# Kernel optimization log

Hardware: AMD Instinct MI355X
Metric: run time of the kernel (lower is better)

Reference implementation:

```python
import jax, jax.numpy as jnp
import numpy as np

# dims: batch, sentences, p/q/a token lens, choices, hidden, selected sentences
B, N, P, Q, A, M, L, K = 32, 32, 64, 32, 24, 4, 768, 2
EPS = 1e-8


def _normalize(x):
    n = jnp.linalg.norm(x, axis=-1, keepdims=True)
    return x / jnp.maximum(n, EPS)


def setup_inputs() -> dict:
    key = jax.random.key(0)
    ks = jax.random.split(key, 16)
    w = lambda k, shape: jax.random.normal(k, shape, jnp.float32) * 0.02
    return {
        "H_p": jax.random.normal(ks[0], (B, N * P, L), jnp.float32),
        "H_q": jax.random.normal(ks[1], (B, Q, L), jnp.float32),
        "H_a": jax.random.normal(ks[2], (B, M * A, L), jnp.float32),
        "W5": w(ks[3], (L, L)),
        "W6": w(ks[4], ((M - 1) * L, L)),
        "W7": w(ks[5], (L, L)),
        "W8": w(ks[6], (L, L)),
        "b8": jnp.zeros((L,), jnp.float32),
        "W9": w(ks[7], (L, L)),
        "W10": w(ks[8], (L, L)),
        "W11": w(ks[9], (L, L)),
        "W12": w(ks[10], (L, L)),
        "W13": w(ks[11], (L, L)),
        "W14": w(ks[12], (L, L)),
        "b14": jnp.zeros((L,), jnp.float32),
        "V": w(ks[13], (3 * L, 1)),
    }


def reference(H_p, H_q, H_a, W5, W6, W7, W8, b8, W9, W10, W11, W12, W13, W14, b14, V):
    Bq = H_q.shape[0]
    Hp = H_p.reshape(Bq, N, P, L)   # (B, N, p, l)
    Ha = H_a.reshape(Bq, M, A, L)   # (B, m, a, l)

    # --- passage sentence selection (cosine scoring) ---
    # The torch code materializes O(B*m*N*a*p*l) repeated tensors; the math is just
    # pairwise cosine similarity -> max over passage tokens -> mean over a/q tokens.
    Pn, An, Qn = _normalize(Hp), _normalize(Ha), _normalize(H_q)
    sim_pa = jnp.einsum('bnpl,bmal->bmnap', Pn, An)  # (B, m, N, a, p)
    score_a = sim_pa.max(-1).mean(-1).sum(1)          # max over p, mean over a, sum over m -> (B, N)
    sim_pq = jnp.einsum('bnpl,bql->bnqp', Pn, Qn)     # (B, N, q, p)
    score_q = sim_pq.max(-1).mean(-1)                 # (B, N)
    score = score_a + score_q
    top_idx = jnp.argsort(-score, axis=-1)[:, :K]     # descending, top-K sentences
    H_p_s = jnp.take_along_axis(Hp, top_idx[:, :, None, None], axis=1).reshape(Bq, K * P, L)

    # --- answer option interaction ---
    H_o = []
    for i in range(M):
        Hi = Ha[:, i]                                  # (B, a, l)
        cache1 = Hi @ W5
        hats = []
        for j in range(M):
            if j != i:
                Hj = Ha[:, j]
                G = jax.nn.softmax(jnp.einsum('bal,bkl->bak', cache1, Hj), axis=-1)
                hats.append(jax.nn.relu(jnp.einsum('bak,bkl->bal', G, Hj)))
        bar = jnp.concatenate(hats, axis=-1) @ W6      # (B, a, l)
        g = jax.nn.sigmoid(bar @ W7 + bar @ W8 + b8)
        H_o.append(g * Hi + (1.0 - g) * bar)
    H_o = jnp.stack(H_o, axis=1)                       # (B, m, a, l)

    # --- bidirectional matching ---
    def match(Hx, Hy, Gxy_left, Gyx_left):
        Gxy = jax.nn.softmax(jnp.einsum('bxl,byl->bxy', Gxy_left, Hy), axis=-1)
        Gyx = jax.nn.softmax(jnp.einsum('byl,bxl->byx', Gyx_left, Hx), axis=-1)
        Ex = jnp.einsum('bxy,byl->bxl', Gxy, Hy)
        Ey = jnp.einsum('byx,bxl->byl', Gyx, Hx)
        Sxy = jax.nn.relu(Ex @ W11).max(1)             # (B, l)
        Syx = jax.nn.relu(Ey @ W12).max(1)             # (B, l)
        g = jax.nn.sigmoid(Sxy @ W13 + Syx @ W14 + b14)
        return g * Sxy + (1.0 - g) * Syx

    cache1 = H_p_s @ W9
    cache2 = H_q @ W9
    cache3 = H_q @ W10
    M_pq = match(H_p_s, H_q, cache1, cache3)
    C = []
    for i in range(M):
        Hoi = H_o[:, i]
        cache4 = Hoi @ W10
        M_po = match(H_p_s, Hoi, cache1, cache4)
        M_qo = match(H_q, Hoi, cache2, cache4)
        C.append(jnp.concatenate([M_pq, M_po, M_qo], axis=-1))
    C = jnp.stack(C, axis=1)                           # (B, m, 3l)
    logits = (C @ V).squeeze(-1)                       # (B, m)
    return jax.nn.log_softmax(logits, axis=-1)
```

## Files before the change

kernel.cpp:

```cpp
#include <hip/hip_runtime.h>
#include <math.h>


typedef __bf16 bf16x8 __attribute__((ext_vector_type(8)));
typedef float f32x4 __attribute__((ext_vector_type(4)));

__global__ void prep_kernel(const float* __restrict__ W5, const float* __restrict__ W6,
                            const float* __restrict__ W7, const float* __restrict__ W8,
                            const float* __restrict__ W9, const float* __restrict__ W10,
                            const float* __restrict__ W11, const float* __restrict__ W12,
                            const float* __restrict__ W13, const float* __restrict__ W14,
                            __bf16* __restrict__ W5t_h, __bf16* __restrict__ W5t_l,
                            __bf16* __restrict__ WsQT_h, __bf16* __restrict__ WsQT_l,
                            __bf16* __restrict__ W6t_h, __bf16* __restrict__ W6t_l,
                            __bf16* __restrict__ W1112T, __bf16* __restrict__ W78t,
                            __bf16* __restrict__ W1314t) {
    long i = (long)blockIdx.x * 256 + threadIdx.x;
    if (i < 589824) {
        int c = (int)(i / 768), r = (int)(i % 768);
        float v = W5[r * 768 + c];
        __bf16 h = (__bf16)v; W5t_h[i] = h; W5t_l[i] = (__bf16)(v - (float)h);
        return;
    } i -= 589824;
    if (i < 1179648) {
        int c = (int)(i / 768), r = (int)(i % 768);
        float v = (c < 768) ? W9[r * 768 + c] : W10[r * 768 + c - 768];
        __bf16 h = (__bf16)v; WsQT_h[i] = h; WsQT_l[i] = (__bf16)(v - (float)h);
        return;
    } i -= 1179648;
    if (i < 1769472) {
        int c = (int)(i / 2304), r = (int)(i % 2304);
        float v = W6[r * 768 + c];
        __bf16 h = (__bf16)v; W6t_h[i] = h; W6t_l[i] = (__bf16)(v - (float)h);
        return;
    } i -= 1769472;
    if (i < 1179648) {
        int c = (int)(i / 768), r = (int)(i % 768);
        W1112T[i] = (__bf16)((c < 768) ? W11[r * 768 + c] : W12[r * 768 + c - 768]);
        return;
    } i -= 1179648;
    if (i < 589824) {
        int c = (int)(i / 768), r = (int)(i % 768);
        W78t[i] = (__bf16)(W7[r * 768 + c] + W8[r * 768 + c]);
        return;
    } i -= 589824;
    if (i < 1179648) {
        int c = (int)(i / 1536), r = (int)(i % 1536);
        W1314t[i] = (__bf16)((r < 768) ? W13[r * 768 + c] : W14[(r - 768) * 768 + c]);
    }
}

__global__ void cvt2_kernel(const float* __restrict__ src, __bf16* __restrict__ h,
                            __bf16* __restrict__ l, long n) {
    long i = (long)blockIdx.x * 256 + threadIdx.x;
    if (i < n) {
        float v = src[i];
        __bf16 hv = (__bf16)v; h[i] = hv; l[i] = (__bf16)(v - (float)hv);
    }
}

__global__ void rnorm_kernel(const float* __restrict__ X, float* __restrict__ out) {
    long row = blockIdx.x;
    const float* xr = X + row * 768;
    int t = threadIdx.x;
    float ss = 0.f;
    for (int l = t; l < 768; l += 256) { float v = xr[l]; ss += v * v; }
    for (int o = 32; o; o >>= 1) ss += __shfl_xor(ss, o);
    __shared__ float red[4];
    if ((t & 63) == 0) red[t >> 6] = ss;
    __syncthreads();
    if (t == 0) {
        float tot = red[0] + red[1] + red[2] + red[3];
        out[row] = 1.f / fmaxf(sqrtf(tot), 1e-8f);
    }
}

__global__ __launch_bounds__(256) void simmax_kernel(
    const float* __restrict__ Hp,
    const __bf16* __restrict__ Ha_h, const __bf16* __restrict__ Ha_l,
    const __bf16* __restrict__ Hq_h, const __bf16* __restrict__ Hq_l,
    const float* __restrict__ ra, const float* __restrict__ rq,
    float* __restrict__ amax) {
    constexpr int LDT = 72;
    __shared__ alignas(16) __bf16 Ah[64 * LDT];
    __shared__ alignas(16) __bf16 Al[64 * LDT];
    __shared__ alignas(16) __bf16 Bh[128 * LDT];
    __shared__ alignas(16) __bf16 Bl[128 * LDT];
    __shared__ float rp_lds[64];
    __shared__ float wred[4][128];
    int b = blockIdx.x >> 5, n = blockIdx.x & 31;
    int t = threadIdx.x;
    const float* Ap = Hp + ((long)b * 2048 + n * 64) * 768;
    int srow = t >> 2, kq = (t & 3) << 4;
    int brow = t >> 1, kh = (t & 1) << 5;
    const __bf16 *Bsh, *Bsl;
    if (brow < 96) {
        Bsh = Ha_h + (long)b * 73728 + (long)brow * 768;
        Bsl = Ha_l + (long)b * 73728 + (long)brow * 768;
    } else {
        Bsh = Hq_h + (long)b * 24576 + (long)(brow - 96) * 768;
        Bsl = Hq_l + (long)b * 24576 + (long)(brow - 96) * 768;
    }
    int w = t >> 6, l = t & 63;
    int fr = l & 15, g = l >> 4;
    int wr = w << 4;
    f32x4 acc[8] = {};
    float ss = 0.f;
    const float* Arow = Ap + (long)srow * 768 + kq;
    for (int k0 = 0; k0 < 768; k0 += 64) {
        float4 av0 = *(const float4*)(Arow + k0 + 0);
        float4 av1 = *(const float4*)(Arow + k0 + 4);
        float4 av2 = *(const float4*)(Arow + k0 + 8);
        float4 av3 = *(const float4*)(Arow + k0 + 12);
        bf16x8 vbh0 = *(const bf16x8*)(Bsh + k0 + kh);
        bf16x8 vbh1 = *(const bf16x8*)(Bsh + k0 + kh + 8);
        bf16x8 vbh2 = *(const bf16x8*)(Bsh + k0 + kh + 16);
        bf16x8 vbh3 = *(const bf16x8*)(Bsh + k0 + kh + 24);
        bf16x8 vbl0 = *(const bf16x8*)(Bsl + k0 + kh);
        bf16x8 vbl1 = *(const bf16x8*)(Bsl + k0 + kh + 8);
        bf16x8 vbl2 = *(const bf16x8*)(Bsl + k0 + kh + 16);
        bf16x8 vbl3 = *(const bf16x8*)(Bsl + k0 + kh + 24);
        float va[16];
        *(float4*)(va + 0) = av0; *(float4*)(va + 4) = av1;
        *(float4*)(va + 8) = av2; *(float4*)(va + 12) = av3;
        bf16x8 h0, h1, l0, l1;
#pragma unroll
        for (int i = 0; i < 8; i++) {
            float v = va[i]; __bf16 hv = (__bf16)v;
            h0[i] = hv; l0[i] = (__bf16)(v - (float)hv); ss += v * v;
            v = va[8 + i]; hv = (__bf16)v;
            h1[i] = hv; l1[i] = (__bf16)(v - (float)hv); ss += v * v;
        }
        __syncthreads();
        *(bf16x8*)(&Ah[srow * LDT + kq]) = h0;
        *(bf16x8*)(&Ah[srow * LDT + kq + 8]) = h1;
        *(bf16x8*)(&Al[srow * LDT + kq]) = l0;
        *(bf16x8*)(&Al[srow * LDT + kq + 8]) = l1;
        *(bf16x8*)(&Bh[brow * LDT + kh]) = vbh0;
        *(bf16x8*)(&Bh[brow * LDT + kh + 8]) = vbh1;
        *(bf16x8*)(&Bh[brow * LDT + kh + 16]) = vbh2;
        *(bf16x8*)(&Bh[brow * LDT + kh + 24]) = vbh3;
        *(bf16x8*)(&Bl[brow * LDT + kh]) = vbl0;
        *(bf16x8*)(&Bl[brow * LDT + kh + 8]) = vbl1;
        *(bf16x8*)(&Bl[brow * LDT + kh + 16]) = vbl2;
        *(bf16x8*)(&Bl[brow * LDT + kh + 24]) = vbl3;
        __syncthreads();
#pragma unroll
        for (int sub = 0; sub < 2; sub++) {
            int kb = sub * 32 + g * 8;
            bf16x8 fah = *(const bf16x8*)(&Ah[(wr + fr) * LDT + kb]);
            bf16x8 fal = *(const bf16x8*)(&Al[(wr + fr) * LDT + kb]);
#pragma unroll
            for (int c = 0; c < 8; c++) {
                bf16x8 fbh = *(const bf16x8*)(&Bh[(c * 16 + fr) * LDT + kb]);
                bf16x8 fbl = *(const bf16x8*)(&Bl[(c * 16 + fr) * LDT + kb]);
                acc[c] = __builtin_amdgcn_mfma_f32_16x16x32_bf16(fah, fbh, acc[c], 0, 0, 0);
                acc[c] = __builtin_amdgcn_mfma_f32_16x16x32_bf16(fah, fbl, acc[c], 0, 0, 0);
                acc[c] = __builtin_amdgcn_mfma_f32_16x16x32_bf16(fal, fbh, acc[c], 0, 0, 0);
            }
        }
    }
    ss += __shfl_xor(ss, 1);
    ss += __shfl_xor(ss, 2);
    if ((t & 3) == 0) rp_lds[srow] = 1.f / fmaxf(sqrtf(ss), 1e-8f);
    __syncthreads();
    float rpv[4];
#pragma unroll
    for (int r = 0; r < 4; r++) rpv[r] = rp_lds[wr + g * 4 + r];
// ... 48 lines not shown
    __bf16 h = (__bf16)v; Hps_h[i] = h; Hps_l[i] = (__bf16)(v - (float)h);
}

template <int BIASF, int BOUT>
__global__ __launch_bounds__(256) void mgemm_kernel(
    const __bf16* __restrict__ A, int Kdim, int Mtot,
    const __bf16* __restrict__ Wt, const float* __restrict__ bias,
    float* __restrict__ C, int ldc, __bf16* __restrict__ Cb) {
    constexpr int LDT = 80;
    __shared__ alignas(16) __bf16 As[64 * LDT];
    __shared__ alignas(16) __bf16 Bs[64 * LDT];
    int t = threadIdx.x;
    int rowBase = blockIdx.x << 6, colBase = blockIdx.y << 6;
    int srow = t >> 2, skof = (t & 3) << 3;
    int arow = rowBase + srow;
    bool aok = arow < Mtot;
    const __bf16* Ap = A + (long)(aok ? arow : rowBase) * Kdim + skof;
    const __bf16* Wp = Wt + (long)(colBase + srow) * Kdim + skof;
    int w = t >> 6, l = t & 63;
    int wr = (w >> 1) << 5, wc = (w & 1) << 5;
    int fr = l & 15, g = l >> 4;
    f32x4 acc[2][2] = {};
    int nk = Kdim >> 6;
    for (int ks = 0; ks < nk; ks++) {
        bf16x8 a0 = *(const bf16x8*)(Ap);
        bf16x8 a1 = *(const bf16x8*)(Ap + 32);
        bf16x8 w0 = *(const bf16x8*)(Wp);
        bf16x8 w1 = *(const bf16x8*)(Wp + 32);
        Ap += 64; Wp += 64;
        __syncthreads();
        *(bf16x8*)(&As[srow * LDT + skof]) = a0;
        *(bf16x8*)(&As[srow * LDT + 32 + skof]) = a1;
        *(bf16x8*)(&Bs[srow * LDT + skof]) = w0;
        *(bf16x8*)(&Bs[srow * LDT + 32 + skof]) = w1;
        __syncthreads();
#pragma unroll
        for (int sub = 0; sub < 2; sub++) {
            int ko = sub * 32 + g * 8;
            bf16x8 fa0 = *(const bf16x8*)(&As[(wr + fr) * LDT + ko]);
            bf16x8 fa1 = *(const bf16x8*)(&As[(wr + 16 + fr) * LDT + ko]);
            bf16x8 fb0 = *(const bf16x8*)(&Bs[(wc + fr) * LDT + ko]);
            bf16x8 fb1 = *(const bf16x8*)(&Bs[(wc + 16 + fr) * LDT + ko]);
            acc[0][0] = __builtin_amdgcn_mfma_f32_16x16x32_bf16(fa0, fb0, acc[0][0], 0, 0, 0);
            acc[0][1] = __builtin_amdgcn_mfma_f32_16x16x32_bf16(fa0, fb1, acc[0][1], 0, 0, 0);
            acc[1][0] = __builtin_amdgcn_mfma_f32_16x16x32_bf16(fa1, fb0, acc[1][0], 0, 0, 0);
            acc[1][1] = __builtin_amdgcn_mfma_f32_16x16x32_bf16(fa1, fb1, acc[1][1], 0, 0, 0);
        }
    }
#pragma unroll
    for (int fi = 0; fi < 2; fi++)
#pragma unroll
    for (int fj = 0; fj < 2; fj++)
#pragma unroll
    for (int r = 0; r < 4; r++) {
        int row = rowBase + wr + fi * 16 + g * 4 + r;
        int col = colBase + wc + fj * 16 + (l & 15);
        if (row < Mtot) {
            float v = acc[fi][fj][r];
            if (BIASF) v += bias[col];
            if (BOUT == 0) C[(long)row * ldc + col] = v;
            else Cb[(long)row * ldc + col] = (__bf16)v;
        }
    }
}

template <int OUT>
__global__ __launch_bounds__(256) void mgemm3_kernel(
    const __bf16* __restrict__ Ah, const __bf16* __restrict__ Al, int Kdim, int Mtot,
    const __bf16* __restrict__ Wh, const __bf16* __restrict__ Wl,
    float* __restrict__ C, int ldc, __bf16* __restrict__ Ch, __bf16* __restrict__ Cl) {
    constexpr int LDT = 80;
    __shared__ alignas(16) __bf16 Ahs[64 * LDT];
    __shared__ alignas(16) __bf16 Als[64 * LDT];
    __shared__ alignas(16) __bf16 Bhs[64 * LDT];
    __shared__ alignas(16) __bf16 Bls[64 * LDT];
    int t = threadIdx.x;
    int rowBase = blockIdx.x << 6, colBase = blockIdx.y << 6;
    int srow = t >> 2, skof = (t & 3) << 3;
    int arow = rowBase + srow;
    bool aok = arow < Mtot;
    long aoff = (long)(aok ? arow : rowBase) * Kdim + skof;
    long woff = (long)(colBase + srow) * Kdim + skof;
    const __bf16* Aph = Ah + aoff;
    const __bf16* Apl = Al + aoff;
    const __bf16* Wph = Wh + woff;
    const __bf16* Wpl = Wl + woff;
    int w = t >> 6, l = t & 63;
    int wr = (w >> 1) << 5, wc = (w & 1) << 5;
    int fr = l & 15, g = l >> 4;
    f32x4 acc[2][2] = {};
    int nk = Kdim >> 6;
    for (int ks = 0; ks < nk; ks++) {
        bf16x8 ah0 = *(const bf16x8*)(Aph);      bf16x8 ah1 = *(const bf16x8*)(Aph + 32);
        bf16x8 al0 = *(const bf16x8*)(Apl);      bf16x8 al1 = *(const bf16x8*)(Apl + 32);
        bf16x8 wh0 = *(const bf16x8*)(Wph);      bf16x8 wh1 = *(const bf16x8*)(Wph + 32);
        bf16x8 wl0 = *(const bf16x8*)(Wpl);      bf16x8 wl1 = *(const bf16x8*)(Wpl + 32);
        Aph += 64; Apl += 64; Wph += 64; Wpl += 64;
        __syncthreads();
        *(bf16x8*)(&Ahs[srow * LDT + skof]) = ah0; *(bf16x8*)(&Ahs[srow * LDT + 32 + skof]) = ah1;
        *(bf16x8*)(&Als[srow * LDT + skof]) = al0; *(bf16x8*)(&Als[srow * LDT + 32 + skof]) = al1;
        *(bf16x8*)(&Bhs[srow * LDT + skof]) = wh0; *(bf16x8*)(&Bhs[srow * LDT + 32 + skof]) = wh1;
        *(bf16x8*)(&Bls[srow * LDT + skof]) = wl0; *(bf16x8*)(&Bls[srow * LDT + 32 + skof]) = wl1;
        __syncthreads();
#pragma unroll
        for (int sub = 0; sub < 2; sub++) {
            int ko = sub * 32 + g * 8;
            bf16x8 fah[2], fal[2], fbh[2], fbl[2];
            fah[0] = *(const bf16x8*)(&Ahs[(wr + fr) * LDT + ko]);
            fah[1] = *(const bf16x8*)(&Ahs[(wr + 16 + fr) * LDT + ko]);
            fal[0] = *(const bf16x8*)(&Als[(wr + fr) * LDT + ko]);
            fal[1] = *(const bf16x8*)(&Als[(wr + 16 + fr) * LDT + ko]);
            fbh[0] = *(const bf16x8*)(&Bhs[(wc + fr) * LDT + ko]);
            fbh[1] = *(const bf16x8*)(&Bhs[(wc + 16 + fr) * LDT + ko]);
            fbl[0] = *(const bf16x8*)(&Bls[(wc + fr) * LDT + ko]);
            fbl[1] = *(const bf16x8*)(&Bls[(wc + 16 + fr) * LDT + ko]);
#pragma unroll
            for (int i = 0; i < 2; i++)
#pragma unroll
            for (int j = 0; j < 2; j++) {
                acc[i][j] = __builtin_amdgcn_mfma_f32_16x16x32_bf16(fah[i], fbh[j], acc[i][j], 0, 0, 0);
                acc[i][j] = __builtin_amdgcn_mfma_f32_16x16x32_bf16(fah[i], fbl[j], acc[i][j], 0, 0, 0);
                acc[i][j] = __builtin_amdgcn_mfma_f32_16x16x32_bf16(fal[i], fbh[j], acc[i][j], 0, 0, 0);
            }
        }
    }
// ... 14 lines not shown
                __bf16 h = (__bf16)v;
                Ch[o] = h; Cl[o] = (__bf16)(v - (float)h);
            }
        }
    }
}

struct QMSeg {
    const __bf16 *GLh, *GLl, *HYh, *HYl;
    float* G;
    int glB, hyB, gB, ldGL, ldHY, shape;
};
struct QMArgs { QMSeg s[18]; };

template <int X, int Y>
__device__ __forceinline__ void qkm_impl(__bf16* SH, float* sc, const QMSeg& sg, int b, int t) {
    constexpr int XR = (X + 15) & ~15;
    constexpr int YR = (Y + 15) & ~15;
    constexpr int LDT = 72;
    constexpr int YC = YR / 16;
    constexpr int F = (XR / 16) * YC;
    constexpr int F4 = F / 4;
    constexpr int YRp = YR + 1;
    __bf16* Ah_ = SH;
    __bf16* Al_ = SH + XR * LDT;
    __bf16* Bh_ = SH + 2 * XR * LDT;
    __bf16* Bl_ = SH + 2 * XR * LDT + YR * LDT;
    int w = t >> 6, l = t & 63, fr = l & 15, g = l >> 4;
    const __bf16* GLbh = sg.GLh + (long)b * sg.glB;
    const __bf16* GLbl = sg.GLl + (long)b * sg.glB;
    const __bf16* HYbh = sg.HYh + (long)b * sg.hyB;
    const __bf16* HYbl = sg.HYl + (long)b * sg.hyB;
    f32x4 acc[F4] = {};
    for (int k0 = 0; k0 < 768; k0 += 64) {
        __syncthreads();
        for (int v = t; v < (XR + YR) * 16; v += 256) {
            int row = v >> 4, sub = v & 15, hl = sub >> 3, k8 = (sub & 7) << 3;
            bf16x8 val = {};
            __bf16* dst;
            if (row < XR) {
                if (row < X)
                    val = *(const bf16x8*)((hl ? GLbl : GLbh) + (long)row * sg.ldGL + k0 + k8);
                dst = (hl ? Al_ : Ah_) + row * LDT + k8;
            } else {
                int r2 = row - XR;
                if (r2 < Y)
                    val = *(const bf16x8*)((hl ? HYbl : HYbh) + (long)r2 * sg.ldHY + k0 + k8);
                dst = (hl ? Bl_ : Bh_) + r2 * LDT + k8;
            }
            *(bf16x8*)dst = val;
        }
        __syncthreads();
#pragma unroll
        for (int sub = 0; sub < 2; sub++) {
            int kb = sub * 32 + g * 8;
#pragma unroll
            for (int ff = 0; ff < F4; ff++) {
                int fidx = w + ff * 4;
                int xm = fidx / YC, yc = fidx % YC;
                bf16x8 fah = *(const bf16x8*)(&Ah_[(xm * 16 + fr) * LDT + kb]);
                bf16x8 fal = *(const bf16x8*)(&Al_[(xm * 16 + fr) * LDT + kb]);
                bf16x8 fbh = *(const bf16x8*)(&Bh_[(yc * 16 + fr) * LDT + kb]);
                bf16x8 fbl = *(const bf16x8*)(&Bl_[(yc * 16 + fr) * LDT + kb]);
                acc[ff] = __builtin_amdgcn_mfma_f32_16x16x32_bf16(fah, fbh, acc[ff], 0, 0, 0);
                acc[ff] = __builtin_amdgcn_mfma_f32_16x16x32_bf16(fah, fbl, acc[ff], 0, 0, 0);
                acc[ff] = __builtin_amdgcn_mfma_f32_16x16x32_bf16(fal, fbh, acc[ff], 0, 0, 0);
            }
        }
    }
#pragma unroll
    for (int ff = 0; ff < F4; ff++) {
        int fidx = w + ff * 4;
        int xm = fidx / YC, yc = fidx % YC;
#pragma unroll
// ... 145 lines not shown
        if (g == 0) {
            int col = n0 + w * 16 + fr;
            sg.outF[(long)b * sg.oB + col] = mx;
            sg.outH[(long)b * sg.oB + col] = (__bf16)mx;
        }
    }
}

__global__ __launch_bounds__(256) void gbm_s_kernel(SArgs2 args) {
    __shared__ alignas(16) __bf16 SH[17408];
    int seg = blockIdx.x >> 5, b = blockIdx.x & 31;
    SSeg2 sg = args.s[seg];
    int t = threadIdx.x;
    switch (sg.shape) {
        case 0: gbm_s_impl<128, 32>(SH, sg, b, t); break;
        case 1: gbm_s_impl<128, 24>(SH, sg, b, t); break;
        case 2: gbm_s_impl<32, 24>(SH, sg, b, t); break;
        case 3: gbm_s_impl<32, 128>(SH, sg, b, t); break;
        case 4: gbm_s_impl<24, 128>(SH, sg, b, t); break;
        default: gbm_s_impl<24, 32>(SH, sg, b, t); break;
    }
}

__global__ void hogate_kernel(const float* __restrict__ gt, const float* __restrict__ bar,
                              const float* __restrict__ Ha,
                              __bf16* __restrict__ Ho_h, __bf16* __restrict__ Ho_l) {
    long idx = (long)blockIdx.x * 256 + threadIdx.x;
    if (idx >= (long)32 * 96 * 768) return;
    float g = 1.f / (1.f + expf(-gt[idx]));
    float v = g * Ha[idx] + (1.f - g) * bar[idx];
    __bf16 h = (__bf16)v; Ho_h[idx] = h; Ho_l[idx] = (__bf16)(v - (float)h);
}

__global__ void logits_kernel(const float* __restrict__ S, const float* __restrict__ gts,
                              const float* __restrict__ V, float* __restrict__ lg) {
    int blk = blockIdx.x; int b = blk >> 2, i = blk & 3;
    int t = threadIdx.x;
    int ms[3] = {0, 1 + i, 5 + i};
    float p = 0.f;
    for (int k = 0; k < 3; k++) {
        int m = ms[k];
        const float* Sr = S + (long)m * 49152 + (long)b * 1536;
        const float* gr = gts + ((long)m * 32 + b) * 768;
        const float* Vr = V + k * 768;
        for (int l = t; l < 768; l += 256) {
            float g = 1.f / (1.f + expf(-gr[l]));
            p += (g * Sr[l] + (1.f - g) * Sr[768 + l]) * Vr[l];
        }
    }
    for (int o = 32; o; o >>= 1) p += __shfl_xor(p, o);
    __shared__ float red[4];
    if ((t & 63) == 0) red[t >> 6] = p;
    __syncthreads();
    if (t == 0) lg[blk] = red[0] + red[1] + red[2] + red[3];
}

__global__ void lsm_kernel(const float* __restrict__ lg, float* __restrict__ out) {
    int b = threadIdx.x;
    if (b >= 32) return;
    float x0 = lg[b * 4 + 0], x1 = lg[b * 4 + 1], x2 = lg[b * 4 + 2], x3 = lg[b * 4 + 3];
    float m = fmaxf(fmaxf(x0, x1), fmaxf(x2, x3));
    float s = expf(x0 - m) + expf(x1 - m) + expf(x2 - m) + expf(x3 - m);
    float ls = m + logf(s);
    out[b * 4 + 0] = x0 - ls; out[b * 4 + 1] = x1 - ls;
    out[b * 4 + 2] = x2 - ls; out[b * 4 + 3] = x3 - ls;
}

extern "C" void kernel_launch(void* const* d_in, const int* in_sizes, int n_in,
                              void* d_out, int out_size, void* d_ws, size_t ws_size,
                              hipStream_t stream) {
    const float* Hp  = (const float*)d_in[0];
    const float* Hq  = (const float*)d_in[1];
    const float* Ha  = (const float*)d_in[2];
    const float* W5  = (const float*)d_in[3];
    const float* W6  = (const float*)d_in[4];
    const float* W7  = (const float*)d_in[5];
    const float* W8  = (const float*)d_in[6];
    const float* b8  = (const float*)d_in[7];
    const float* W9  = (const float*)d_in[8];
    const float* W10 = (const float*)d_in[9];
    const float* W11 = (const float*)d_in[10];
    const float* W12 = (const float*)d_in[11];
    const float* W13 = (const float*)d_in[12];
    const float* W14 = (const float*)d_in[13];
    const float* b14 = (const float*)d_in[14];
    const float* V   = (const float*)d_in[15];
    float* out = (float*)d_out;
    (void)in_sizes; (void)n_in; (void)out_size; (void)ws_size;

    char* base = (char*)d_ws;
    size_t off = 0;
    auto take = [&](size_t bytes) { char* p = base + off; off += (bytes + 15) & ~15UL; return p; };

    __bf16* W5t_h  = (__bf16*)take(1179648);
    __bf16* W5t_l  = (__bf16*)take(1179648);
    __bf16* WsQT_h = (__bf16*)take(2359296);
    __bf16* WsQT_l = (__bf16*)take(2359296);
    __bf16* W6t_h  = (__bf16*)take(3538944);
    __bf16* W6t_l  = (__bf16*)take(3538944);
    __bf16* W1112T = (__bf16*)take(2359296);
    __bf16* W78t   = (__bf16*)take(1179648);
    __bf16* W1314t = (__bf16*)take(2359296);
    float* ra     = (float*)take(12288);
    float* rq     = (float*)take(4096);
    float* amax   = (float*)take(524288);
    int*   topidx = (int*)take(256);
    float* lg     = (float*)take(512);
    __bf16* Ha_h  = (__bf16*)take(4718592);
    __bf16* Ha_l  = (__bf16*)take(4718592);
    __bf16* Hq_h  = (__bf16*)take(1572864);
    __bf16* Hq_l  = (__bf16*)take(1572864);
    __bf16* Hps_h = (__bf16*)take(6291456);
    __bf16* Hps_l = (__bf16*)take(6291456);
    __bf16* C1_h  = (__bf16*)take(4718592);
    __bf16* C1_l  = (__bf16*)take(4718592);
    __bf16* HqS_h = (__bf16*)take(3145728);
    __bf16* HqS_l = (__bf16*)take(3145728);
    __bf16* c1_h  = (__bf16*)take(6291456);
    __bf16* c1_l  = (__bf16*)take(6291456);
    __bf16* c4_h  = (__bf16*)take(4718592);
    __bf16* c4_l  = (__bf16*)take(4718592);
    __bf16* Ho_h  = (__bf16*)take(4718592);
    __bf16* Ho_l  = (__bf16*)take(4718592);
    __bf16* hats_h = (__bf16*)take(14155776);
    __bf16* hats_l = (__bf16*)take(14155776);
    __bf16* bar_h  = (__bf16*)take(4718592);
    __bf16* HqS2_bf   = (__bf16*)take(3145728);
    __bf16* HpsW12_bf = (__bf16*)take(6291456);
    __bf16* HoW11_bf  = (__bf16*)take(4718592);
    __bf16* S_h    = (__bf16*)take(884736);
    float* bar  = (float*)take(9437184);
    float* gt   = (float*)take(9437184);
    float* G2   = (float*)take(884736);
    float* Gm   = (float*)take(5111808);
    float* S    = (float*)take(1769472);
    float* gts  = (float*)take(884736);

    dim3 blk(256);

    prep_kernel<<<25344, blk, 0, stream>>>(W5, W6, W7, W8, W9, W10, W11, W12, W13, W14,
                                           W5t_h, W5t_l, WsQT_h, WsQT_l, W6t_h, W6t_l,
                                           W1112T, W78t, W1314t);
    cvt2_kernel<<<9216, blk, 0, stream>>>(Ha, Ha_h, Ha_l, 2359296);
    cvt2_kernel<<<3072, blk, 0, stream>>>(Hq, Hq_h, Hq_l, 786432);

    rnorm_kernel<<<3072, blk, 0, stream>>>(Ha, ra);
    rnorm_kernel<<<1024, blk, 0, stream>>>(Hq, rq);
    simmax_kernel<<<1024, blk, 0, stream>>>(Hp, Ha_h, Ha_l, Hq_h, Hq_l, ra, rq, amax);
    score_top2_kernel<<<32, dim3(64), 0, stream>>>(amax, topidx);
    gather_kernel<<<12288, blk, 0, stream>>>(Hp, topidx, Hps_h, Hps_l);

    mgemm3_kernel<2><<<dim3(48, 12), blk, 0, stream>>>(Ha_h, Ha_l, 768, 3072, W5t_h, W5t_l, nullptr, 768, C1_h, C1_l);
    mgemm3_kernel<2><<<dim3(16, 24), blk, 0, stream>>>(Hq_h, Hq_l, 768, 1024, WsQT_h, WsQT_l, nullptr, 1536, HqS_h, HqS_l);
    mgemm3_kernel<2><<<dim3(64, 12), blk, 0, stream>>>(Hps_h, Hps_l, 768, 4096, WsQT_h, WsQT_l, nullptr, 768, c1_h, c1_l);
    mgemm_kernel<0, 1><<<dim3(16, 24), blk, 0, stream>>>(Hq_h, 768, 1024, W1112T, nullptr, nullptr, 1536, HqS2_bf);
    mgemm_kernel<0, 1><<<dim3(64, 12), blk, 0, stream>>>(Hps_h, 768, 4096, W1112T + (long)768 * 768, nullptr, nullptr, 768, HpsW12_bf);

    {
        QMArgs qa{}; int si = 0;
        for (int i = 0; i < 4; i++)
            for (int j = 0; j < 4; j++) {
                if (j == i) continue;
                QMSeg& s = qa.s[si];
                s.GLh = C1_h + (long)i * 24 * 768; s.GLl = C1_l + (long)i * 24 * 768;
                s.HYh = Ha_h + (long)j * 24 * 768; s.HYl = Ha_l + (long)j * 24 * 768;
                s.G = G2 + (long)si * 18432;
                s.glB = 73728; s.hyB = 73728; s.gB = 576;
                s.ldGL = 768; s.ldHY = 768; s.shape = 0;
                si++;
            }
        qkm_kernel<<<12 * 32, blk, 0, stream>>>(qa);
    }
    {
        HArgs ha{}; int si = 0;
        for (int i = 0; i < 4; i++) {
            int jj = 0;
            for (int j = 0; j < 4; j++) {
                if (j == i) continue;
                HSeg& s = ha.s[si];
                s.G = G2 + (long)si * 18432; s.gB = 576;
                s.Bh = Ha_h + (long)j * 24 * 768; s.Bl = Ha_l + (long)j * 24 * 768; s.bB = 73728;
                s.outH = hats_h + (long)i * 24 * 2304 + jj * 768;
                s.outL = hats_l + (long)i * 24 * 2304 + jj * 768;
                s.oB = 221184;
                si++; jj++;
            }
        }
        gbm_hats_kernel<<<12 * 32, blk, 0, stream>>>(ha);
    }
    mgemm3_kernel<1><<<dim3(48, 12), blk, 0, stream>>>(hats_h, hats_l, 2304, 3072, W6t_h, W6t_l, bar, 768, bar_h, nullptr);
    mgemm_kernel<1, 0><<<dim3(48, 12), blk, 0, stream>>>(bar_h, 768, 3072, W78t, b8, gt, 768, nullptr);
    hogate_kernel<<<9216, blk, 0, stream>>>(gt, bar, Ha, Ho_h, Ho_l);
    mgemm3_kernel<2><<<dim3(48, 12), blk, 0, stream>>>(Ho_h, Ho_l, 768, 3072, WsQT_h + (long)768 * 768, WsQT_l + (long)768 * 768, nullptr, 768, c4_h, c4_l);
    mgemm_kernel<0, 1><<<dim3(48, 12), blk, 0, stream>>>(Ho_h, 768, 3072, W1112T, nullptr, nullptr, 768, HoW11_bf);

    const long gA0 = 0, gA1 = 131072, gA5 = 524288, gA9 = 622592, gB0 = 720896, gB1 = 851968;

    {
        QMArgs qa{};
        auto set = [&](int k, const __bf16* GLh, const __bf16* GLl, int glB, int ldGL,
                       const __bf16* HYh, const __bf16* HYl, int hyB, int ldHY,
                       float* G, int gB, int shape) {
            QMSeg& s = qa.s[k];
            s.GLh = GLh; s.GLl = GLl; s.HYh = HYh; s.HYl = HYl; s.G = G;
            s.glB = glB; s.hyB = hyB; s.gB = gB; s.ldGL = ldGL; s.ldHY = ldHY; s.shape = shape;
        };
        set(0, c1_h, c1_l, 98304, 768, Hq_h, Hq_l, 24576, 768, Gm + gA0, 4096, 1);
        for (int i = 0; i < 4; i++) {
            set(1 + i, c1_h, c1_l, 98304, 768,
                Ho_h + (long)i * 24 * 768, Ho_l + (long)i * 24 * 768, 73728, 768,
                Gm + gA1 + (long)i * 98304, 3072, 2);
            set(5 + i, HqS_h, HqS_l, 49152, 1536,
                Ho_h + (long)i * 24 * 768, Ho_l + (long)i * 24 * 768, 73728, 768,
                Gm + gA5 + (long)i * 24576, 768, 3);
            set(9 + i, c4_h + (long)i * 24 * 768, c4_l + (long)i * 24 * 768, 73728, 768,
// ... 14 lines not shown
            SSeg2& s = sa.s[k];
            s.G = G; s.gB = gB; s.B = Bp; s.bB = bB; s.ldB = ldB;
            s.outF = oF; s.outH = oH; s.oB = 1536; s.shape = shape;
        };
        set(0, Gm + gA0, 4096, HqS2_bf, 49152, 1536, S, S_h, 0);
        for (int i = 0; i < 4; i++) {
            set(1 + i, Gm + gA1 + (long)i * 98304, 3072, HoW11_bf + (long)i * 24 * 768, 73728, 768,
                S + (long)(1 + i) * 49152, S_h + (long)(1 + i) * 49152, 1);
            set(5 + i, Gm + gA5 + (long)i * 24576, 768, HoW11_bf + (long)i * 24 * 768, 73728, 768,
                S + (long)(5 + i) * 49152, S_h + (long)(5 + i) * 49152, 2);
        }
        set(9, Gm + gB0, 4096, HpsW12_bf, 98304, 768, S + 768, S_h + 768, 3);
        for (int i = 0; i < 4; i++) {
            set(10 + i, Gm + gB1 + (long)i * 98304, 3072, HpsW12_bf, 98304, 768,
                S + (long)(1 + i) * 49152 + 768, S_h + (long)(1 + i) * 49152 + 768, 4);
            set(14 + i, Gm + gA9 + (long)i * 24576, 768, HqS2_bf + 768, 49152, 1536,
                S + (long)(5 + i) * 49152 + 768, S_h + (long)(5 + i) * 49152 + 768, 5);
        }
        gbm_s_kernel<<<18 * 32, blk, 0, stream>>>(sa);
    }

    mgemm_kernel<1, 0><<<dim3(5, 12), blk, 0, stream>>>(S_h, 1536, 288, W1314t, b14, gts, 768, nullptr);

    logits_kernel<<<128, blk, 0, stream>>>(S, gts, V, lg);
    lsm_kernel<<<1, dim3(32), 0, stream>>>(lg, out);
}
```

Before: 536.8 us.

## Tile-transpose weight prep, fuse conversions, prefetch GEMM loads, fuse gate and logits

Weight preparation now transposes through 32x32 shared-memory tiles, so the strided uncoalesced reads are replaced by coalesced ones. The bf16 hi/lo conversion and row-norm kernels are merged into one pass, and the sigmoid gate is fused into the W7+W8 GEMM epilogue, which removes the gt buffer and the hogate kernel. Logits and log-softmax become a single kernel. Several GEMM loops (simmax, mgemm, mgemm3, the QM kernel) register-prefetch the next K tile while the current one is written to shared memory, at the cost of extra registers.

```diff
diff --git a/kernel.cpp b/kernel.cpp
--- a/kernel.cpp
+++ b/kernel.cpp
@@ -5,74 +5,85 @@
 typedef __bf16 bf16x8 __attribute__((ext_vector_type(8)));
 typedef float f32x4 __attribute__((ext_vector_type(4)));
 
-__global__ void prep_kernel(const float* __restrict__ W5, const float* __restrict__ W6,
-                            const float* __restrict__ W7, const float* __restrict__ W8,
-                            const float* __restrict__ W9, const float* __restrict__ W10,
-                            const float* __restrict__ W11, const float* __restrict__ W12,
-                            const float* __restrict__ W13, const float* __restrict__ W14,
-                            __bf16* __restrict__ W5t_h, __bf16* __restrict__ W5t_l,
-                            __bf16* __restrict__ WsQT_h, __bf16* __restrict__ WsQT_l,
-                            __bf16* __restrict__ W6t_h, __bf16* __restrict__ W6t_l,
-                            __bf16* __restrict__ W1112T, __bf16* __restrict__ W78t,
-                            __bf16* __restrict__ W1314t) {
-    long i = (long)blockIdx.x * 256 + threadIdx.x;
-    if (i < 589824) {
-        int c = (int)(i / 768), r = (int)(i % 768);
-        float v = W5[r * 768 + c];
-        __bf16 h = (__bf16)v; W5t_h[i] = h; W5t_l[i] = (__bf16)(v - (float)h);
-        return;
-    } i -= 589824;
-    if (i < 1179648) {
-        int c = (int)(i / 768), r = (int)(i % 768);
-        float v = (c < 768) ? W9[r * 768 + c] : W10[r * 768 + c - 768];
-        __bf16 h = (__bf16)v; WsQT_h[i] = h; WsQT_l[i] = (__bf16)(v - (float)h);
-        return;
-    } i -= 1179648;
-    if (i < 1769472) {
-        int c = (int)(i / 2304), r = (int)(i % 2304);
-        float v = W6[r * 768 + c];
-        __bf16 h = (__bf16)v; W6t_h[i] = h; W6t_l[i] = (__bf16)(v - (float)h);
-        return;
-    } i -= 1769472;
-    if (i < 1179648) {
-        int c = (int)(i / 768), r = (int)(i % 768);
-        W1112T[i] = (__bf16)((c < 768) ? W11[r * 768 + c] : W12[r * 768 + c - 768]);
-        return;
-    } i -= 1179648;
-    if (i < 589824) {
-        int c = (int)(i / 768), r = (int)(i % 768);
-        W78t[i] = (__bf16)(W7[r * 768 + c] + W8[r * 768 + c]);
-        return;
-    } i -= 589824;
-    if (i < 1179648) {
-        int c = (int)(i / 1536), r = (int)(i % 1536);
-        W1314t[i] = (__bf16)((r < 768) ? W13[r * 768 + c] : W14[(r - 768) * 768 + c]);
-    }
-}
-
-__global__ void cvt2_kernel(const float* __restrict__ src, __bf16* __restrict__ h,
-                            __bf16* __restrict__ l, long n) {
-    long i = (long)blockIdx.x * 256 + threadIdx.x;
-    if (i < n) {
-        float v = src[i];
-        __bf16 hv = (__bf16)v; h[i] = hv; l[i] = (__bf16)(v - (float)hv);
-    }
-}
-
-__global__ void rnorm_kernel(const float* __restrict__ X, float* __restrict__ out) {
+__global__ __launch_bounds__(256) void prep_kernel(
+    const float* __restrict__ W5, const float* __restrict__ W6,
+    const float* __restrict__ W7, const float* __restrict__ W8,
+    const float* __restrict__ W9, const float* __restrict__ W10,
+    const float* __restrict__ W11, const float* __restrict__ W12,
+    const float* __restrict__ W13, const float* __restrict__ W14,
+    __bf16* __restrict__ W5t_h, __bf16* __restrict__ W5t_l,
+    __bf16* __restrict__ WsQT_h, __bf16* __restrict__ WsQT_l,
+    __bf16* __restrict__ W6t_h, __bf16* __restrict__ W6t_l,
+    __bf16* __restrict__ W1112T, __bf16* __restrict__ W78t,
+    __bf16* __restrict__ W1314t) {
+    __shared__ float T[32][33];
+    int blk = blockIdx.x;
+    int job, rel;
+    if (blk < 576) { job = 0; rel = blk; }
+    else if (blk < 1728) { job = 1; rel = blk - 576; }
+    else if (blk < 3456) { job = 2; rel = blk - 1728; }
+    else if (blk < 4608) { job = 3; rel = blk - 3456; }
+    else if (blk < 5184) { job = 4; rel = blk - 4608; }
+    else { job = 5; rel = blk - 5184; }
+    int KT = (job == 2) ? 72 : (job == 5) ? 48 : 24;
+    int Kdim = KT * 32;
+    int ntile = rel / KT, ktile = rel - ntile * KT;
+    int k0 = ktile * 32, n0 = ntile * 32;
+    int t = threadIdx.x, tx = t & 31, ty = t >> 5;
+#pragma unroll
+    for (int s = 0; s < 4; s++) {
+        int k = k0 + ty + 8 * s;
+        int n = n0 + tx;
+        float v;
+        switch (job) {
+            case 0: v = W5[(long)k * 768 + n]; break;
+            case 1: v = (n < 768) ? W9[(long)k * 768 + n] : W10[(long)k * 768 + n - 768]; break;
+            case 2: v = W6[(long)k * 768 + n]; break;
+            case 3: v = (n < 768) ? W11[(long)k * 768 + n] : W12[(long)k * 768 + n - 768]; break;
+            case 4: v = W7[(long)k * 768 + n] + W8[(long)k * 768 + n]; break;
+            default: v = (k < 768) ? W13[(long)k * 768 + n] : W14[(long)(k - 768) * 768 + n]; break;
+        }
+        T[ty + 8 * s][tx] = v;
+    }
+    __syncthreads();
+#pragma unroll
+    for (int s = 0; s < 4; s++) {
+        int n = n0 + ty + 8 * s;
+        int k = k0 + tx;
+        float v = T[tx][ty + 8 * s];
+        long o = (long)n * Kdim + k;
+        __bf16 h = (__bf16)v;
+        switch (job) {
+            case 0: W5t_h[o] = h; W5t_l[o] = (__bf16)(v - (float)h); break;
+            case 1: WsQT_h[o] = h; WsQT_l[o] = (__bf16)(v - (float)h); break;
+            case 2: W6t_h[o] = h; W6t_l[o] = (__bf16)(v - (float)h); break;
+            case 3: W1112T[o] = h; break;
+            case 4: W78t[o] = h; break;
+            default: W1314t[o] = h; break;
+        }
+    }
+}
+
+__global__ __launch_bounds__(256) void cvt2n_kernel(const float* __restrict__ src,
+                                                    __bf16* __restrict__ h, __bf16* __restrict__ l,
+                                                    float* __restrict__ rn) {
     long row = blockIdx.x;
-    const float* xr = X + row * 768;
     int t = threadIdx.x;
+    const float* sr = src + row * 768;
     float ss = 0.f;
-    for (int l = t; l < 768; l += 256) { float v = xr[l]; ss += v * v; }
+#pragma unroll
+    for (int i = 0; i < 3; i++) {
+        int idx = t + i * 256;
+        float v = sr[idx];
+        __bf16 hv = (__bf16)v;
+        h[row * 768 + idx] = hv; l[row * 768 + idx] = (__bf16)(v - (float)hv);
+        ss += v * v;
+    }
     for (int o = 32; o; o >>= 1) ss += __shfl_xor(ss, o);
     __shared__ float red[4];
     if ((t & 63) == 0) red[t >> 6] = ss;
     __syncthreads();
-    if (t == 0) {
-        float tot = red[0] + red[1] + red[2] + red[3];
-        out[row] = 1.f / fmaxf(sqrtf(tot), 1e-8f);
-    }
+    if (t == 0) rn[row] = 1.f / fmaxf(sqrtf(red[0] + red[1] + red[2] + red[3]), 1e-8f);
 }
 
 __global__ __launch_bounds__(256) void simmax_kernel(
@@ -107,19 +118,24 @@
     f32x4 acc[8] = {};
     float ss = 0.f;
     const float* Arow = Ap + (long)srow * 768 + kq;
+    float4 av0, av1, av2, av3;
+    bf16x8 vbh0, vbh1, vbh2, vbh3, vbl0, vbl1, vbl2, vbl3;
+    auto LOADS = [&](int k0) {
+        av0 = *(const float4*)(Arow + k0 + 0);
+        av1 = *(const float4*)(Arow + k0 + 4);
+        av2 = *(const float4*)(Arow + k0 + 8);
+        av3 = *(const float4*)(Arow + k0 + 12);
+        vbh0 = *(const bf16x8*)(Bsh + k0 + kh);
+        vbh1 = *(const bf16x8*)(Bsh + k0 + kh + 8);
+        vbh2 = *(const bf16x8*)(Bsh + k0 + kh + 16);
+        vbh3 = *(const bf16x8*)(Bsh + k0 + kh + 24);
+        vbl0 = *(const bf16x8*)(Bsl + k0 + kh);
+        vbl1 = *(const bf16x8*)(Bsl + k0 + kh + 8);
+        vbl2 = *(const bf16x8*)(Bsl + k0 + kh + 16);
+        vbl3 = *(const bf16x8*)(Bsl + k0 + kh + 24);
+    };
+    LOADS(0);
     for (int k0 = 0; k0 < 768; k0 += 64) {
-        float4 av0 = *(const float4*)(Arow + k0 + 0);
-        float4 av1 = *(const float4*)(Arow + k0 + 4);
-        float4 av2 = *(const float4*)(Arow + k0 + 8);
-        float4 av3 = *(const float4*)(Arow + k0 + 12);
-        bf16x8 vbh0 = *(const bf16x8*)(Bsh + k0 + kh);
-        bf16x8 vbh1 = *(const bf16x8*)(Bsh + k0 + kh + 8);
-        bf16x8 vbh2 = *(const bf16x8*)(Bsh + k0 + kh + 16);
-        bf16x8 vbh3 = *(const bf16x8*)(Bsh + k0 + kh + 24);
-        bf16x8 vbl0 = *(const bf16x8*)(Bsl + k0 + kh);
-        bf16x8 vbl1 = *(const bf16x8*)(Bsl + k0 + kh + 8);
-        bf16x8 vbl2 = *(const bf16x8*)(Bsl + k0 + kh + 16);
-        bf16x8 vbl3 = *(const bf16x8*)(Bsl + k0 + kh + 24);
         float va[16];
         *(float4*)(va + 0) = av0; *(float4*)(va + 4) = av1;
         *(float4*)(va + 8) = av2; *(float4*)(va + 12) = av3;
@@ -131,19 +147,22 @@
             v = va[8 + i]; hv = (__bf16)v;
             h1[i] = hv; l1[i] = (__bf16)(v - (float)hv); ss += v * v;
         }
+        bf16x8 sbh0 = vbh0, sbh1 = vbh1, sbh2 = vbh2, sbh3 = vbh3;
+        bf16x8 sbl0 = vbl0, sbl1 = vbl1, sbl2 = vbl2, sbl3 = vbl3;
         __syncthreads();
         *(bf16x8*)(&Ah[srow * LDT + kq]) = h0;
         *(bf16x8*)(&Ah[srow * LDT + kq + 8]) = h1;
         *(bf16x8*)(&Al[srow * LDT + kq]) = l0;
         *(bf16x8*)(&Al[srow * LDT + kq + 8]) = l1;
-        *(bf16x8*)(&Bh[brow * LDT + kh]) = vbh0;
-        *(bf16x8*)(&Bh[brow * LDT + kh + 8]) = vbh1;
-        *(bf16x8*)(&Bh[brow * LDT + kh + 16]) = vbh2;
-        *(bf16x8*)(&Bh[brow * LDT + kh + 24]) = vbh3;
-        *(bf16x8*)(&Bl[brow * LDT + kh]) = vbl0;
-        *(bf16x8*)(&Bl[brow * LDT + kh + 8]) = vbl1;
-        *(bf16x8*)(&Bl[brow * LDT + kh + 16]) = vbl2;
-        *(bf16x8*)(&Bl[brow * LDT + kh + 24]) = vbl3;
+        *(bf16x8*)(&Bh[brow * LDT + kh]) = sbh0;
+        *(bf16x8*)(&Bh[brow * LDT + kh + 8]) = sbh1;
+        *(bf16x8*)(&Bh[brow * LDT + kh + 16]) = sbh2;
+        *(bf16x8*)(&Bh[brow * LDT + kh + 24]) = sbh3;
+        *(bf16x8*)(&Bl[brow * LDT + kh]) = sbl0;
+        *(bf16x8*)(&Bl[brow * LDT + kh + 8]) = sbl1;
+        *(bf16x8*)(&Bl[brow * LDT + kh + 16]) = sbl2;
+        *(bf16x8*)(&Bl[brow * LDT + kh + 24]) = sbl3;
+        if (k0 + 64 < 768) LOADS(k0 + 64);
         __syncthreads();
 #pragma unroll
         for (int sub = 0; sub < 2; sub++) {
@@ -238,17 +257,20 @@
     int fr = l & 15, g = l >> 4;
     f32x4 acc[2][2] = {};
     int nk = Kdim >> 6;
+    bf16x8 a0, a1, w0, w1;
+    auto LOADM = [&]() {
+        a0 = *(const bf16x8*)(Ap); a1 = *(const bf16x8*)(Ap + 32);
+        w0 = *(const bf16x8*)(Wp); w1 = *(const bf16x8*)(Wp + 32);
+        Ap += 64; Wp += 64;
+    };
+    LOADM();
     for (int ks = 0; ks < nk; ks++) {
-        bf16x8 a0 = *(const bf16x8*)(Ap);
-        bf16x8 a1 = *(const bf16x8*)(Ap + 32);
-        bf16x8 w0 = *(const bf16x8*)(Wp);
-        bf16x8 w1 = *(const bf16x8*)(Wp + 32);
-        Ap += 64; Wp += 64;
         __syncthreads();
         *(bf16x8*)(&As[srow * LDT + skof]) = a0;
         *(bf16x8*)(&As[srow * LDT + 32 + skof]) = a1;
         *(bf16x8*)(&Bs[srow * LDT + skof]) = w0;
         *(bf16x8*)(&Bs[srow * LDT + 32 + skof]) = w1;
+        if (ks + 1 < nk) LOADM();
         __syncthreads();
 #pragma unroll
         for (int sub = 0; sub < 2; sub++) {
@@ -277,6 +299,68 @@
             if (BOUT == 0) C[(long)row * ldc + col] = v;
             else Cb[(long)row * ldc + col] = (__bf16)v;
         }
+    }
+}
+
+__global__ __launch_bounds__(256) void mgemm_gate_kernel(
+    const __bf16* __restrict__ A, const __bf16* __restrict__ Wt, const float* __restrict__ bias,
+    const float* __restrict__ HaF, const float* __restrict__ barF,
+    __bf16* __restrict__ Ho_h, __bf16* __restrict__ Ho_l) {
+    constexpr int LDT = 80;
+    constexpr int Kdim = 768;
+    __shared__ alignas(16) __bf16 As[64 * LDT];
+    __shared__ alignas(16) __bf16 Bs[64 * LDT];
+    int t = threadIdx.x;
+    int rowBase = blockIdx.x << 6, colBase = blockIdx.y << 6;
+    int srow = t >> 2, skof = (t & 3) << 3;
+    const __bf16* Ap = A + (long)(rowBase + srow) * Kdim + skof;
+    const __bf16* Wp = Wt + (long)(colBase + srow) * Kdim + skof;
+    int w = t >> 6, l = t & 63;
+    int wr = (w >> 1) << 5, wc = (w & 1) << 5;
+    int fr = l & 15, g = l >> 4;
+    f32x4 acc[2][2] = {};
+    bf16x8 a0, a1, w0, w1;
+    auto LOADM = [&]() {
+        a0 = *(const bf16x8*)(Ap); a1 = *(const bf16x8*)(Ap + 32);
+        w0 = *(const bf16x8*)(Wp); w1 = *(const bf16x8*)(Wp + 32);
+        Ap += 64; Wp += 64;
+    };
+    LOADM();
+    for (int ks = 0; ks < 12; ks++) {
+        __syncthreads();
+        *(bf16x8*)(&As[srow * LDT + skof]) = a0;
+        *(bf16x8*)(&As[srow * LDT + 32 + skof]) = a1;
+        *(bf16x8*)(&Bs[srow * LDT + skof]) = w0;
+        *(bf16x8*)(&Bs[srow * LDT + 32 + skof]) = w1;
+        if (ks + 1 < 12) LOADM();
+        __syncthreads();
+#pragma unroll
+        for (int sub = 0; sub < 2; sub++) {
+            int ko = sub * 32 + g * 8;
+            bf16x8 fa0 = *(const bf16x8*)(&As[(wr + fr) * LDT + ko]);
+            bf16x8 fa1 = *(const bf16x8*)(&As[(wr + 16 + fr) * LDT + ko]);
+            bf16x8 fb0 = *(const bf16x8*)(&Bs[(wc + fr) * LDT + ko]);
+            bf16x8 fb1 = *(const bf16x8*)(&Bs[(wc + 16 + fr) * LDT + ko]);
+            acc[0][0] = __builtin_amdgcn_mfma_f32_16x16x32_bf16(fa0, fb0, acc[0][0], 0, 0, 0);
+            acc[0][1] = __builtin_amdgcn_mfma_f32_16x16x32_bf16(fa0, fb1, acc[0][1], 0, 0, 0);
+            acc[1][0] = __builtin_amdgcn_mfma_f32_16x16x32_bf16(fa1, fb0, acc[1][0], 0, 0, 0);
+            acc[1][1] = __builtin_amdgcn_mfma_f32_16x16x32_bf16(fa1, fb1, acc[1][1], 0, 0, 0);
+        }
+    }
+#pragma unroll
+    for (int fi = 0; fi < 2; fi++)
+#pragma unroll
+    for (int fj = 0; fj < 2; fj++)
+#pragma unroll
+    for (int r = 0; r < 4; r++) {
+        int row = rowBase + wr + fi * 16 + g * 4 + r;
+        int col = colBase + wc + fj * 16 + (l & 15);
+        float v = acc[fi][fj][r] + bias[col];
+        float gt = 1.f / (1.f + expf(-v));
+        long o = (long)row * 768 + col;
+        float hv = gt * HaF[o] + (1.f - gt) * barF[o];
+        __bf16 hb = (__bf16)hv;
+        Ho_h[o] = hb; Ho_l[o] = (__bf16)(hv - (float)hb);
     }
 }
 
@@ -306,17 +390,22 @@
     int fr = l & 15, g = l >> 4;
     f32x4 acc[2][2] = {};
     int nk = Kdim >> 6;
+    bf16x8 ah0, ah1, al0, al1, wh0, wh1, wl0, wl1;
+    auto LOADM = [&]() {
+        ah0 = *(const bf16x8*)(Aph); ah1 = *(const bf16x8*)(Aph + 32);
+        al0 = *(const bf16x8*)(Apl); al1 = *(const bf16x8*)(Apl + 32);
+        wh0 = *(const bf16x8*)(Wph); wh1 = *(const bf16x8*)(Wph + 32);
+        wl0 = *(const bf16x8*)(Wpl); wl1 = *(const bf16x8*)(Wpl + 32);
+        Aph += 64; Apl += 64; Wph += 64; Wpl += 64;
+    };
+    LOADM();
     for (int ks = 0; ks < nk; ks++) {
-        bf16x8 ah0 = *(const bf16x8*)(Aph);      bf16x8 ah1 = *(const bf16x8*)(Aph + 32);
-        bf16x8 al0 = *(const bf16x8*)(Apl);      bf16x8 al1 = *(const bf16x8*)(Apl + 32);
-        bf16x8 wh0 = *(const bf16x8*)(Wph);      bf16x8 wh1 = *(const bf16x8*)(Wph + 32);
-        bf16x8 wl0 = *(const bf16x8*)(Wpl);      bf16x8 wl1 = *(const bf16x8*)(Wpl + 32);
-        Aph += 64; Apl += 64; Wph += 64; Wpl += 64;
         __syncthreads();
         *(bf16x8*)(&Ahs[srow * LDT + skof]) = ah0; *(bf16x8*)(&Ahs[srow * LDT + 32 + skof]) = ah1;
         *(bf16x8*)(&Als[srow * LDT + skof]) = al0; *(bf16x8*)(&Als[srow * LDT + 32 + skof]) = al1;
         *(bf16x8*)(&Bhs[srow * LDT + skof]) = wh0; *(bf16x8*)(&Bhs[srow * LDT + 32 + skof]) = wh1;
         *(bf16x8*)(&Bls[srow * LDT + skof]) = wl0; *(bf16x8*)(&Bls[srow * LDT + 32 + skof]) = wl1;
+        if (ks + 1 < nk) LOADM();
         __syncthreads();
 #pragma unroll
         for (int sub = 0; sub < 2; sub++) {
@@ -377,6 +466,7 @@
     constexpr int F = (XR / 16) * YC;
     constexpr int F4 = F / 4;
     constexpr int YRp = YR + 1;
+    constexpr int NST = (XR + YR) * 16 / 256;
     __bf16* Ah_ = SH;
     __bf16* Al_ = SH + XR * LDT;
     __bf16* Bh_ = SH + 2 * XR * LDT;
@@ -387,24 +477,37 @@
     const __bf16* HYbh = sg.HYh + (long)b * sg.hyB;
     const __bf16* HYbl = sg.HYl + (long)b * sg.hyB;
     f32x4 acc[F4] = {};
-    for (int k0 = 0; k0 < 768; k0 += 64) {
-        __syncthreads();
-        for (int v = t; v < (XR + YR) * 16; v += 256) {
+    bf16x8 stg[NST];
+    auto LOADQ = [&](int k0) {
+#pragma unroll
+        for (int s = 0; s < NST; s++) {
+            int v = t + s * 256;
             int row = v >> 4, sub = v & 15, hl = sub >> 3, k8 = (sub & 7) << 3;
             bf16x8 val = {};
-            __bf16* dst;
             if (row < XR) {
                 if (row < X)
                     val = *(const bf16x8*)((hl ? GLbl : GLbh) + (long)row * sg.ldGL + k0 + k8);
-                dst = (hl ? Al_ : Ah_) + row * LDT + k8;
             } else {
                 int r2 = row - XR;
                 if (r2 < Y)
                     val = *(const bf16x8*)((hl ? HYbl : HYbh) + (long)r2 * sg.ldHY + k0 + k8);
-                dst = (hl ? Bl_ : Bh_) + r2 * LDT + k8;
             }
-            *(bf16x8*)dst = val;
-        }
+            stg[s] = val;
+        }
+    };
+    LOADQ(0);
+    for (int k0 = 0; k0 < 768; k0 += 64) {
+        __syncthreads();
+#pragma unroll
+        for (int s = 0; s < NST; s++) {
+            int v = t + s * 256;
+            int row = v >> 4, sub = v & 15, hl = sub >> 3, k8 = (sub & 7) << 3;
+            __bf16* dst;
+            if (row < XR) dst = (hl ? Al_ : Ah_) + row * LDT + k8;
+            else dst = (hl ? Bl_ : Bh_) + (row - XR) * LDT + k8;
+            *(bf16x8*)dst = stg[s];
+        }
+        if (k0 + 64 < 768) LOADQ(k0 + 64);
         __syncthreads();
 #pragma unroll
         for (int sub = 0; sub < 2; sub++) {
@@ -596,20 +699,11 @@
     }
 }
 
-__global__ void hogate_kernel(const float* __restrict__ gt, const float* __restrict__ bar,
-                              const float* __restrict__ Ha,
-                              __bf16* __restrict__ Ho_h, __bf16* __restrict__ Ho_l) {
-    long idx = (long)blockIdx.x * 256 + threadIdx.x;
-    if (idx >= (long)32 * 96 * 768) return;
-    float g = 1.f / (1.f + expf(-gt[idx]));
-    float v = g * Ha[idx] + (1.f - g) * bar[idx];
-    __bf16 h = (__bf16)v; Ho_h[idx] = h; Ho_l[idx] = (__bf16)(v - (float)h);
-}
-
-__global__ void logits_kernel(const float* __restrict__ S, const float* __restrict__ gts,
-                              const float* __restrict__ V, float* __restrict__ lg) {
-    int blk = blockIdx.x; int b = blk >> 2, i = blk & 3;
-    int t = threadIdx.x;
+__global__ __launch_bounds__(256) void logits_lsm_kernel(
+    const float* __restrict__ S, const float* __restrict__ gts,
+    const float* __restrict__ V, float* __restrict__ out) {
+    int b = blockIdx.x;
+    int t = threadIdx.x, i = t >> 6, lane = t & 63;
     int ms[3] = {0, 1 + i, 5 + i};
     float p = 0.f;
     for (int k = 0; k < 3; k++) {
@@ -617,27 +711,23 @@
         const float* Sr = S + (long)m * 49152 + (long)b * 1536;
         const float* gr = gts + ((long)m * 32 + b) * 768;
         const float* Vr = V + k * 768;
-        for (int l = t; l < 768; l += 256) {
+        for (int l = lane; l < 768; l += 64) {
             float g = 1.f / (1.f + expf(-gr[l]));
             p += (g * Sr[l] + (1.f - g) * Sr[768 + l]) * Vr[l];
         }
     }
     for (int o = 32; o; o >>= 1) p += __shfl_xor(p, o);
-    __shared__ float red[4];
-    if ((t & 63) == 0) red[t >> 6] = p;
+    __shared__ float lgs[4];
+    if (lane == 0) lgs[i] = p;
     __syncthreads();
-    if (t == 0) lg[blk] = red[0] + red[1] + red[2] + red[3];
-}
-
-__global__ void lsm_kernel(const float* __restrict__ lg, float* __restrict__ out) {
-    int b = threadIdx.x;
-    if (b >= 32) return;
-    float x0 = lg[b * 4 + 0], x1 = lg[b * 4 + 1], x2 = lg[b * 4 + 2], x3 = lg[b * 4 + 3];
-    float m = fmaxf(fmaxf(x0, x1), fmaxf(x2, x3));
-    float s = expf(x0 - m) + expf(x1 - m) + expf(x2 - m) + expf(x3 - m);
-    float ls = m + logf(s);
-    out[b * 4 + 0] = x0 - ls; out[b * 4 + 1] = x1 - ls;
-    out[b * 4 + 2] = x2 - ls; out[b * 4 + 3] = x3 - ls;
+    if (t == 0) {
+        float x0 = lgs[0], x1 = lgs[1], x2 = lgs[2], x3 = lgs[3];
+        float m = fmaxf(fmaxf(x0, x1), fmaxf(x2, x3));
+        float s = expf(x0 - m) + expf(x1 - m) + expf(x2 - m) + expf(x3 - m);
+        float ls = m + logf(s);
+        out[b * 4 + 0] = x0 - ls; out[b * 4 + 1] = x1 - ls;
+        out[b * 4 + 2] = x2 - ls; out[b * 4 + 3] = x3 - ls;
+    }
 }
 
 extern "C" void kernel_launch(void* const* d_in, const int* in_sizes, int n_in,
@@ -679,7 +769,6 @@
     float* rq     = (float*)take(4096);
     float* amax   = (float*)take(524288);
     int*   topidx = (int*)take(256);
-    float* lg     = (float*)take(512);
     __bf16* Ha_h  = (__bf16*)take(4718592);
     __bf16* Ha_l  = (__bf16*)take(4718592);
     __bf16* Hq_h  = (__bf16*)take(1572864);
@@ -704,7 +793,6 @@
     __bf16* HoW11_bf  = (__bf16*)take(4718592);
     __bf16* S_h    = (__bf16*)take(884736);
     float* bar  = (float*)take(9437184);
-    float* gt   = (float*)take(9437184);
     float* G2   = (float*)take(884736);
     float* Gm   = (float*)take(5111808);
     float* S    = (float*)take(1769472);
@@ -712,14 +800,12 @@
 
     dim3 blk(256);
 
-    prep_kernel<<<25344, blk, 0, stream>>>(W5, W6, W7, W8, W9, W10, W11, W12, W13, W14,
-                                           W5t_h, W5t_l, WsQT_h, WsQT_l, W6t_h, W6t_l,
-                                           W1112T, W78t, W1314t);
-    cvt2_kernel<<<9216, blk, 0, stream>>>(Ha, Ha_h, Ha_l, 2359296);
-    cvt2_kernel<<<3072, blk, 0, stream>>>(Hq, Hq_h, Hq_l, 786432);
-
-    rnorm_kernel<<<3072, blk, 0, stream>>>(Ha, ra);
-    rnorm_kernel<<<1024, blk, 0, stream>>>(Hq, rq);
+    prep_kernel<<<6336, blk, 0, stream>>>(W5, W6, W7, W8, W9, W10, W11, W12, W13, W14,
+                                          W5t_h, W5t_l, WsQT_h, WsQT_l, W6t_h, W6t_l,
+                                          W1112T, W78t, W1314t);
+    cvt2n_kernel<<<3072, blk, 0, stream>>>(Ha, Ha_h, Ha_l, ra);
+    cvt2n_kernel<<<1024, blk, 0, stream>>>(Hq, Hq_h, Hq_l, rq);
+
     simmax_kernel<<<1024, blk, 0, stream>>>(Hp, Ha_h, Ha_l, Hq_h, Hq_l, ra, rq, amax);
     score_top2_kernel<<<32, dim3(64), 0, stream>>>(amax, topidx);
     gather_kernel<<<12288, blk, 0, stream>>>(Hp, topidx, Hps_h, Hps_l);
@@ -763,8 +849,7 @@
         gbm_hats_kernel<<<12 * 32, blk, 0, stream>>>(ha);
     }
     mgemm3_kernel<1><<<dim3(48, 12), blk, 0, stream>>>(hats_h, hats_l, 2304, 3072, W6t_h, W6t_l, bar, 768, bar_h, nullptr);
-    mgemm_kernel<1, 0><<<dim3(48, 12), blk, 0, stream>>>(bar_h, 768, 3072, W78t, b8, gt, 768, nullptr);
-    hogate_kernel<<<9216, blk, 0, stream>>>(gt, bar, Ha, Ho_h, Ho_l);
+    mgemm_gate_kernel<<<dim3(48, 12), blk, 0, stream>>>(bar_h, W78t, b8, Ha, bar, Ho_h, Ho_l);
     mgemm3_kernel<2><<<dim3(48, 12), blk, 0, stream>>>(Ho_h, Ho_l, 768, 3072, WsQT_h + (long)768 * 768, WsQT_l + (long)768 * 768, nullptr, 768, c4_h, c4_l);
     mgemm_kernel<0, 1><<<dim3(48, 12), blk, 0, stream>>>(Ho_h, 768, 3072, W1112T, nullptr, nullptr, 768, HoW11_bf);
 
@@ -825,6 +910,5 @@
 
     mgemm_kernel<1, 0><<<dim3(5, 12), blk, 0, stream>>>(S_h, 1536, 288, W1314t, b14, gts, 768, nullptr);
 
-    logits_kernel<<<128, blk, 0, stream>>>(S, gts, V, lg);
-    lsm_kernel<<<1, dim3(32), 0, stream>>>(lg, out);
-}
+    logits_lsm_kernel<<<32, blk, 0, stream>>>(S, gts, V, out);
+}
```

New measurement: 646.5 us. 20.4% more time.
